# Optimization experiments

Measured on AMD Instinct MI355X. Metric: run time of the kernel, lower is better.

The kernel has to match this reference:

```python
import jax, jax.numpy as jnp
import numpy as np

NORMAL, INFLOW, OUTFLOW, WALL, PRESS_POINT = 0, 4, 5, 6, 7
NX = NY = 1024


def setup_inputs() -> dict:
    Ex, Ey = NX + 2, NY + 2
    n = NX * NY
    n_ext = Ex * Ey
    oidx = np.arange(n); io = oidx % NX; jo = oidx // NX
    nt = np.zeros(n, np.int32)
    nt[jo == 0] = WALL; nt[jo == NY - 1] = WALL
    nt[io == 0] = INFLOW; nt[io == NX - 1] = OUTFLOW
    e = np.arange(n_ext); ie = e % Ex; je = e // Ex
    extend_index = (np.clip(je - 1, 0, NY - 1) * NX + np.clip(ie - 1, 0, NX - 1)).astype(np.int32)
    ent = nt[extend_index].copy()
    ent[je == 0] = WALL; ent[je == Ey - 1] = WALL
    ent[ie == 0] = INFLOW; ent[ie == Ex - 1] = OUTFLOW
    ent[(Ey // 2) * Ex + Ex // 2] = PRESS_POINT
    jr = np.arange(1, Ey - 1); ir = np.arange(1, Ex - 1)
    ghost = np.concatenate([
        np.stack([jr * Ex, jr * Ex + 1, jr * Ex + 2], 1),
        np.stack([jr * Ex + Ex - 1, jr * Ex + Ex - 2, jr * Ex + Ex - 3], 1),
        np.stack([ir, Ex + ir, 2 * Ex + ir], 1),
        np.stack([(Ey - 1) * Ex + ir, (Ey - 2) * Ex + ir, (Ey - 3) * Ex + ir], 1)], 0).astype(np.int32)
    fx = np.arange((Ex - 1) * Ey); fxi = fx % (Ex - 1); fxj = fx // (Ex - 1)
    edge_node_xi = np.stack([fxj * Ex + fxi, fxj * Ex + fxi + 1], 0).astype(np.int32)
    fy = np.arange(Ex * (Ey - 1)); fyi = fy % Ex; fyj = fy // Ex
    edge_node_eta = np.stack([fyj * Ex + fyi, (fyj + 1) * Ex + fyi], 0).astype(np.int32)
    ie0 = io + 1; je0 = jo + 1
    xi_face = np.stack([je0 * (Ex - 1) + ie0 - 1, je0 * (Ex - 1) + ie0], 0).astype(np.int32)
    eta_face = np.stack([(je0 - 1) * Ex + ie0, je0 * Ex + ie0], 0).astype(np.int32)
    c = np.arange((Ex - 1) * (Ey - 1)); ci = c % (Ex - 1); cj = c // (Ex - 1)
    block_cells_node = np.stack([cj * Ex + ci, cj * Ex + ci + 1, (cj + 1) * Ex + ci, (cj + 1) * Ex + ci + 1], 0).astype(np.int32)
    xi_cell_index = np.stack([fyj * (Ex - 1) + np.clip(fyi - 1, 0, Ex - 2), fyj * (Ex - 1) + np.clip(fyi, 0, Ex - 2)], 0).astype(np.int32)
    key = jax.random.key(0)
    k = jax.random.split(key, 8)
    m0 = 1.0 + 0.05 * jax.random.normal(k[0], (n_ext,))
    m1 = 0.05 * jax.random.normal(k[1], (n_ext,))
    m2 = 0.05 * jax.random.normal(k[2], (n_ext,))
    m3 = 1.0 + 0.05 * jax.random.normal(k[3], (n_ext,))
    Jm = m0 * m3 - m1 * m2
    ebm = jnp.stack([m0, m1, m2, m3, Jm], 1)
    interior = (jo + 1) * Ex + (io + 1)
    obm = ebm[interior]
    return {
        "original_uv": 0.1 * jax.random.normal(k[4], (n, 3)),
        "uv_old": 0.1 * jax.random.normal(k[5], (n, 3)),
        "node_y": 0.1 * jax.random.normal(k[6], (n, 3)),
        "original_block_metrics": obm,
        "extended_block_metrics": ebm,
        "dt_graph": jnp.full((1, 1), 0.01, jnp.float32),
        "pde_theta": 0.5 + jax.random.uniform(k[7], (1, 5)),
        "relaxtion": jnp.full((1, 1), 0.5, jnp.float32),
        "node_type": jnp.asarray(nt),
        "ext_node_type": jnp.asarray(ent),
        "extend_index": jnp.asarray(extend_index),
        "ghost_stencil": jnp.asarray(ghost),
        "block_cells_node": jnp.asarray(block_cells_node),
        "edge_node_xi": jnp.asarray(edge_node_xi),
        "edge_node_eta": jnp.asarray(edge_node_eta),
        "xi_face": jnp.asarray(xi_face),
        "eta_face": jnp.asarray(eta_face),
        "xi_cell_index": jnp.asarray(xi_cell_index),
        "batch": jnp.zeros((n,), jnp.int32),
    }


def _hard_enforce_bc(uvp, node_type, node_y, extend_index, ext_node_type, ghost):
    mask_bc = (node_type == INFLOW) | (node_type == WALL)
    out_mask = node_type == OUTFLOW
    dummy_uv = jnp.where(mask_bc[:, None], node_y[:, :2], uvp[:, :2])
    dummy_p = jnp.where(out_mask, 0.0, uvp[:, 2])
    dummy = jnp.concatenate([dummy_uv, dummy_p[:, None]], 1)
    dummy_ext = dummy[extend_index]
    ext = uvp[extend_index]
    g0, g1, g2 = ghost[:, 0], ghost[:, 1], ghost[:, 2]
    gt = ext_node_type[g0]
    uvmask = gt == OUTFLOW
    pmask = (gt == WALL) | (gt == INFLOW)
    new_uv = jnp.where(pmask[:, None], 2.0 * dummy_ext[g1, :2] - ext[g2, :2],
                       jnp.where(uvmask[:, None], ext[g2, :2], ext[g0, :2]))
    new_p = jnp.where(uvmask, 2.0 * dummy_ext[g1, 2] - ext[g2, 2],
                      jnp.where(pmask, ext[g2, 2], ext[g0, 2]))
    return ext.at[g0, :2].set(new_uv).at[g0, 2].set(new_p)


def _convect_flux(uv, dxx, dxy, dex, dey, Jm, ln, rn, dn, un, le, re, de, ue):
    U = (uv[:, 0] * dxx + uv[:, 1] * dxy) / Jm
    V = (uv[:, 0] * dex + uv[:, 1] * dey) / Jm
    U_face = 0.5 * (U[ln] + U[rn]); V_face = 0.5 * (V[dn] + V[un])
    uv_xi = 0.5 * (uv[ln] + uv[rn]); uv_eta = 0.5 * (uv[dn] + uv[un])
    d1 = uv_xi[re] * U_face[re][:, None] - uv_xi[le] * U_face[le][:, None]
    d2 = uv_eta[ue] * V_face[ue][:, None] - uv_eta[de] * V_face[de][:, None]
    return jnp.concatenate([d1, d2], 1)  # [n,4]: dE1u,dE1v,dE2u,dE2v


def _diffuse_flux(uv, dxx, dxy, dex, dey, Jm, ln, rn, dn, un, le, re, de, ue):
    # central second-difference viscous flux in curvilinear coords (orthogonal terms)
    a11 = (dxx * dxx + dxy * dxy) / Jm
    a22 = (dex * dex + dey * dey) / Jm
    fx = (0.5 * (a11[ln] + a11[rn]))[:, None] * (uv[rn] - uv[ln])
    fy = (0.5 * (a22[dn] + a22[un]))[:, None] * (uv[un] - uv[dn])
    return jnp.concatenate([fx[re] - fx[le], fy[ue] - fy[de]], 1)


def _forward(original_uv, uv_old, node_y, obm, ebm, dt_graph, pde_theta, relaxtion,
             node_type, ext_node_type, extend_index, ghost_stencil, block_cells_node,
             edge_node_xi, edge_node_eta, xi_face, eta_face, xi_cell_index, batch):
    ext_old = _hard_enforce_bc(uv_old, node_type, node_y, extend_index, ext_node_type, ghost_stencil)
    ext = _hard_enforce_bc(original_uv, node_type, node_y, extend_index, ext_node_type, ghost_stencil)
    press = ext_node_type == PRESS_POINT
    ext = ext.at[:, 2].set(jnp.where(press, 0.0, ext[:, 2]))
    dxx, dxy, dex, dey, Jm = ebm[:, 0], ebm[:, 1], ebm[:, 2], ebm[:, 3], ebm[:, 4]
    J_o = obm[:, 4]
    ln, rn = edge_node_xi[0], edge_node_xi[1]
    dn, un = edge_node_eta[0], edge_node_eta[1]
    le, re = xi_face[0], xi_face[1]
    de, ue = eta_face[0], eta_face[1]
    lc, rc = xi_cell_index[0], xi_cell_index[1]
    dt_node = dt_graph[batch]            # [n,1]
    theta = pde_theta[batch]             # [n,5]
    uc, cc, convc, pc, dc = theta[:, 0:1], theta[:, 1:2], theta[:, 2:3], theta[:, 3:4], theta[:, 4:5]
    relax = relaxtion[batch]             # [n,1]
    uvc = ext[:, :2]; p = ext[:, 2]
    # continuity
    U = (uvc[:, 0] * dxx + uvc[:, 1] * dxy) / Jm
    V = (uvc[:, 0] * dex + uvc[:, 1] * dey) / Jm
    U_face = 0.5 * (U[ln] + U[rn]); V_face = 0.5 * (V[dn] + V[un])
    loss_cont = (U_face[re] - U_face[le] + V_face[ue] - V_face[de])[:, None] * cc
    conv_old = _convect_flux(ext_old[:, :2], dxx, dxy, dex, dey, Jm, ln, rn, dn, un, le, re, de, ue)
    conv_new = _convect_flux(uvc, dxx, dxy, dex, dey, Jm, ln, rn, dn, un, le, re, de, ue)
    diff_new = _diffuse_flux(uvc, dxx, dxy, dex, dey, Jm, ln, rn, dn, un, le, re, de, ue)
    conv = conv_old * relax + conv_new * (1.0 - relax)
    dE1u, dE1v, dE2u, dE2v = conv[:, 0], conv[:, 1], conv[:, 2], conv[:, 3]
    dv1u, dv1v, dv2u, dv2v = diff_new[:, 0], diff_new[:, 1], diff_new[:, 2], diff_new[:, 3]
    # pressure gradient
    pq = p / Jm
    pxx = pq * dxx; pxy = pq * dxy; pex = pq * dex; pey = pq * dey
    pxx_f = 0.5 * (pxx[ln] + pxx[rn]); pxy_f = 0.5 * (pxy[ln] + pxy[rn])
    pex_f = 0.5 * (pex[dn] + pex[un]); pey_f = 0.5 * (pey[dn] + pey[un])
    gPx = pxx_f[re] - pxx_f[le] + pex_f[ue] - pex_f[de]
    gPy = pey_f[ue] - pey_f[de] + pxy_f[re] - pxy_f[le]
    convect = jnp.stack([dE1u + dE2u, dE1v + dE2v], 1)
    diffusion = jnp.stack([dv1u + dv2u, dv1v + dv2v], 1)
    unsteady = (original_uv[:, :2] - uv_old[:, :2]) / dt_node / J_o[:, None]
    grad_P = jnp.stack([gPx, gPy], 1)
    momentum = uc * unsteady + convc * convect + pc * grad_P - dc * diffusion
    # smooth=True visualization field
    cell_uvp = 0.25 * (ext[block_cells_node[0]] + ext[block_cells_node[1]] + ext[block_cells_node[2]] + ext[block_cells_node[3]])
    face_eta = 0.5 * (cell_uvp[lc] + cell_uvp[rc])
    uvp_to_vis = jax.lax.stop_gradient(0.5 * (face_eta[ue] + face_eta[de]))
    return loss_cont, momentum[:, 0:1], momentum[:, 1:2], uvp_to_vis


def reference(original_uv, uv_old, node_y, original_block_metrics, extended_block_metrics,
              dt_graph, pde_theta, relaxtion, node_type, ext_node_type, extend_index,
              ghost_stencil, block_cells_node, edge_node_xi, edge_node_eta, xi_face,
              eta_face, xi_cell_index, batch):
    return _forward(original_uv, uv_old, node_y, original_block_metrics, extended_block_metrics,
                    dt_graph, pde_theta, relaxtion, node_type, ext_node_type, extend_index,
                    ghost_stencil, block_cells_node, edge_node_xi, edge_node_eta, xi_face,
                    eta_face, xi_cell_index, batch)
```

## Files before the change

kernel.cpp:

```cpp
#include <hip/hip_runtime.h>


#define NXC 1024
#define EXC 1026
#define NN  (NXC*NXC)

enum { T_NORMAL=0, T_INFLOW=4, T_OUTFLOW=5, T_WALL=6, T_PRESS=7 };

struct V3 { float u,v,p; };

__device__ __forceinline__ int ntype(int io,int jo){
  if (io==NXC-1) return T_OUTFLOW;
  if (io==0)     return T_INFLOW;
  if (jo==0 || jo==NXC-1) return T_WALL;
  return T_NORMAL;
}

template<bool NEWF>
__device__ __forceinline__ V3 ext_at(int je,int ie,
    const float* __restrict__ uvp,
    const float* __restrict__ node_y)
{
  V3 r;
  const bool bl=(ie==0), br=(ie==EXC-1), bb=(je==0), bt=(je==EXC-1);
  const bool onx = bl||br, ony = bb||bt;
  const bool ghost = (onx && !ony) || (ony && !onx);
  if (!ghost){
    int io = ie-1; io = io<0?0:(io>NXC-1?NXC-1:io);
    int jo = je-1; jo = jo<0?0:(jo>NXC-1?NXC-1:jo);
    int m3 = 3*(jo*NXC+io);
    r.u = uvp[m3]; r.v = uvp[m3+1]; r.p = uvp[m3+2];
    if (NEWF && je==EXC/2 && ie==EXC/2) r.p = 0.f;
    return r;
  }
  int dje=0, die=0, gt;
  if (bl)      { die= 1; gt=T_INFLOW;  }
  else if (br) { die=-1; gt=T_OUTFLOW; }
  else if (bb) { dje= 1; gt=T_WALL;    }
  else         { dje=-1; gt=T_WALL;    }
  int io1 = ie+die-1, jo1 = je+dje-1;
  int m1 = 3*(jo1*NXC+io1);
  int m2 = 3*((jo1+dje)*NXC + (io1+die));
  float u2=uvp[m2], v2=uvp[m2+1], p2=uvp[m2+2];
  int nt1 = ntype(io1,jo1);
  if (gt==T_OUTFLOW){
    float p1 = (nt1==T_OUTFLOW) ? 0.f : uvp[m1+2];
    r.u=u2; r.v=v2; r.p = 2.f*p1 - p2;
  } else {
    float du,dv;
    if (nt1==T_INFLOW || nt1==T_WALL){ du=node_y[m1]; dv=node_y[m1+1]; }
    else                             { du=uvp[m1];    dv=uvp[m1+1];    }
    r.u = 2.f*du - u2; r.v = 2.f*dv - v2; r.p = p2;
  }
  return r;
}

__device__ void process_slow(int io,int jo,
    const float* __restrict__ uvp, const float* __restrict__ uvo,
    const float* __restrict__ ndy, const float* __restrict__ ebm,
    float dt,float uc,float cc,float convc,float pc,float dc,float relax,
    float* __restrict__ out)
{
  const int o = jo*NXC + io;
  const int ie0 = io+1, je0 = jo+1;
  V3 C  = ext_at<true >(je0,  ie0,  uvp, ndy);
  V3 W  = ext_at<true >(je0,  ie0-1,uvp, ndy);
  V3 E  = ext_at<true >(je0,  ie0+1,uvp, ndy);
  V3 S  = ext_at<true >(je0-1,ie0,  uvp, ndy);
  V3 Nn = ext_at<true >(je0+1,ie0,  uvp, ndy);
  V3 SW = ext_at<true >(je0-1,ie0-1,uvp, ndy);
  V3 SE = ext_at<true >(je0-1,ie0+1,uvp, ndy);
  V3 NW = ext_at<true >(je0+1,ie0-1,uvp, ndy);
  V3 NE = ext_at<true >(je0+1,ie0+1,uvp, ndy);
  V3 Co = ext_at<false>(je0,  ie0,  uvo, ndy);
  V3 Wo = ext_at<false>(je0,  ie0-1,uvo, ndy);
  V3 Eo = ext_at<false>(je0,  ie0+1,uvo, ndy);
  V3 So = ext_at<false>(je0-1,ie0,  uvo, ndy);
  V3 No = ext_at<false>(je0+1,ie0,  uvo, ndy);

  const int eC = je0*EXC+ie0;
  const int eW = eC-1, eE = eC+1, eS = eC-EXC, eN = eC+EXC;
  float dxxC=ebm[5*eC+0], dxyC=ebm[5*eC+1], dexC=ebm[5*eC+2],
        deyC=ebm[5*eC+3], JmC=ebm[5*eC+4];
  float dxxW=ebm[5*eW+0], dxyW=ebm[5*eW+1], JmW=ebm[5*eW+4];
  float dxxE=ebm[5*eE+0], dxyE=ebm[5*eE+1], JmE=ebm[5*eE+4];
  float dexS=ebm[5*eS+2], deyS=ebm[5*eS+3], JmS=ebm[5*eS+4];
  float dexN=ebm[5*eN+2], deyN=ebm[5*eN+3], JmN=ebm[5*eN+4];
  const float rC=1.f/JmC, rW=1.f/JmW, rE=1.f/JmE, rS=1.f/JmS, rN=1.f/JmN;

  float UC=(C.u*dxxC + C.v*dxyC)*rC, UW=(W.u*dxxW + W.v*dxyW)*rW, UE=(E.u*dxxE + E.v*dxyE)*rE;
  float VC=(C.u*dexC + C.v*deyC)*rC, VS=(S.u*dexS + S.v*deyS)*rS, VN=(Nn.u*dexN + Nn.v*deyN)*rN;
  float UCo=(Co.u*dxxC + Co.v*dxyC)*rC, UWo=(Wo.u*dxxW + Wo.v*dxyW)*rW, UEo=(Eo.u*dxxE + Eo.v*dxyE)*rE;
  float VCo=(Co.u*dexC + Co.v*deyC)*rC, VSo=(So.u*dexS + So.v*deyS)*rS, VNo=(No.u*dexN + No.v*deyN)*rN;

  float Ufl =0.5f*(UW +UC ), Ufr =0.5f*(UC +UE );
  float Vfd =0.5f*(VS +VC ), Vfu =0.5f*(VC +VN );
  float Uflo=0.5f*(UWo+UCo), Ufro=0.5f*(UCo+UEo);
  float Vfdo=0.5f*(VSo+VCo), Vfuo=0.5f*(VCo+VNo);

  const float loss = (Ufr - Ufl + Vfu - Vfd) * cc;

  float cnu = 0.5f*(C.u+E.u)*Ufr - 0.5f*(W.u+C.u)*Ufl + 0.5f*(C.u+Nn.u)*Vfu - 0.5f*(S.u+C.u)*Vfd;
  float cnv = 0.5f*(C.v+E.v)*Ufr - 0.5f*(W.v+C.v)*Ufl + 0.5f*(C.v+Nn.v)*Vfu - 0.5f*(S.v+C.v)*Vfd;
  float cou = 0.5f*(Co.u+Eo.u)*Ufro - 0.5f*(Wo.u+Co.u)*Uflo + 0.5f*(Co.u+No.u)*Vfuo - 0.5f*(So.u+Co.u)*Vfdo;
  float cov = 0.5f*(Co.v+Eo.v)*Ufro - 0.5f*(Wo.v+Co.v)*Uflo + 0.5f*(Co.v+No.v)*Vfuo - 0.5f*(So.v+Co.v)*Vfdo;
  const float convu = relax*cou + (1.f-relax)*cnu;
  const float convv = relax*cov + (1.f-relax)*cnv;

  float a11C=(dxxC*dxxC+dxyC*dxyC)*rC, a11W=(dxxW*dxxW+dxyW*dxyW)*rW, a11E=(dxxE*dxxE+dxyE*dxyE)*rE;
  float a22C=(dexC*dexC+deyC*deyC)*rC, a22S=(dexS*dexS+deyS*deyS)*rS, a22N=(dexN*dexN+deyN*deyN)*rN;
  float du = 0.5f*(a11C+a11E)*(E.u -C.u) - 0.5f*(a11W+a11C)*(C.u-W.u)
           + 0.5f*(a22C+a22N)*(Nn.u-C.u) - 0.5f*(a22S+a22C)*(C.u-S.u);
  float dv = 0.5f*(a11C+a11E)*(E.v -C.v) - 0.5f*(a11W+a11C)*(C.v-W.v)
           + 0.5f*(a22C+a22N)*(Nn.v-C.v) - 0.5f*(a22S+a22C)*(C.v-S.v);

  float pqW=W.p*rW, pqE=E.p*rE, pqS=S.p*rS, pqN=Nn.p*rN;
  const float gPx = 0.5f*(pqE*dxxE - pqW*dxxW) + 0.5f*(pqN*dexN - pqS*dexS);
  const float gPy = 0.5f*(pqN*deyN - pqS*deyS) + 0.5f*(pqE*dxyE - pqW*dxyW);

  const float rdt = 1.f/dt;
  const float unst_u = (C.u - Co.u)*rdt*rC;
  const float unst_v = (C.v - Co.v)*rdt*rC;

  const float momu = uc*unst_u + convc*convu + pc*gPx - dc*du;
  const float momv = uc*unst_v + convc*convv + pc*gPy - dc*dv;

  const float visu = (SW.u+SE.u+NW.u+NE.u + 2.f*(S.u+W.u+E.u+Nn.u) + 4.f*C.u)*0.0625f;
  const float visv = (SW.v+SE.v+NW.v+NE.v + 2.f*(S.v+W.v+E.v+Nn.v) + 4.f*C.v)*0.0625f;
  const float visp = (SW.p+SE.p+NW.p+NE.p + 2.f*(S.p+W.p+E.p+Nn.p) + 4.f*C.p)*0.0625f;

  out[o]        = loss;
  out[NN + o]   = momu;
  out[2*NN + o] = momv;
  const int vb = 3*NN + 3*o;
  out[vb]   = visu;
  out[vb+1] = visv;
  out[vb+2] = visp;
}

extern "C" __global__ void __launch_bounds__(512)
fd_kernel(const float* __restrict__ uvp,
          const float* __restrict__ uvo,
          const float* __restrict__ ndy,
          const float* __restrict__ ebm,
          const float* __restrict__ dtg,
          const float* __restrict__ th,
          const float* __restrict__ rl,
          float* __restrict__ out)
{
  const int jo = blockIdx.x;
  int t = threadIdx.x;
  int s = (t==63) ? 511 : ((t==511) ? 63 : t);
  const int x0 = s*2;

  const float dt   = dtg[0];
  const float uc   = th[0], cc = th[1], convc = th[2], pc = th[3], dc = th[4];
  const float relax= rl[0];
  const float rdt  = 1.f/dt;

  const bool edge = (x0==0) | (x0==NXC-2) | (jo==0) | (jo==NXC-1);
  if (edge){
    process_slow(x0,  jo, uvp,uvo,ndy,ebm, dt,uc,cc,convc,pc,dc,relax, out);
    process_slow(x0+1,jo, uvp,uvo,ndy,ebm, dt,uc,cc,convc,pc,dc,relax, out);
    return;
  }

  const int rm=jo-1, rc=jo, rp=jo+1;

  float nS[12], nC[12], nN[12];
  {
    const float* a = uvp + 3*(rm*NXC + x0-1);
    const float* b = uvp + 3*(rc*NXC + x0-1);
    const float* c = uvp + 3*(rp*NXC + x0-1);
    #pragma unroll
    for (int k=0;k<12;k++){ nS[k]=a[k]; nC[k]=b[k]; nN[k]=c[k]; }
  }
  float qS[6], qC[12], qN[6];
  {
    const float* a = uvo + 3*(rm*NXC + x0);
    const float* b = uvo + 3*(rc*NXC + x0-1);
    const float* c = uvo + 3*(rp*NXC + x0);
    #pragma unroll
    for (int k=0;k<6;k++){ qS[k]=a[k]; qN[k]=c[k]; }
    #pragma unroll
    for (int k=0;k<12;k++){ qC[k]=b[k]; }
  }
  float mc[20], ms[10], mn[10];
  {
    const float* a = ebm + 5*((jo  )*EXC + x0+1);
    const float* b = ebm + 5*((jo+1)*EXC + x0);
    const float* c = ebm + 5*((jo+2)*EXC + x0+1);
    #pragma unroll
    for (int k=0;k<10;k++){ ms[k]=a[k]; mn[k]=c[k]; }
    #pragma unroll
    for (int k=0;k<20;k++){ mc[k]=b[k]; }
  }

  {
    const int c = 513 - x0;
    if ((unsigned)c < 4u){
      if (rm==512) nS[3*c+2]=0.f;
      if (rc==512) nC[3*c+2]=0.f;
      if (rp==512) nN[3*c+2]=0.f;
    }
  }

  float Un[4],Uo[4],a11[4],pqx[4],pqy[4],rJ[4],dex_[4],dey_[4];
  #pragma unroll
  for (int k=0;k<4;k++){
    const float dxx=mc[5*k], dxy=mc[5*k+1];
    dex_[k]=mc[5*k+2]; dey_[k]=mc[5*k+3];
    rJ[k]=1.f/mc[5*k+4];
    Un[k]=(nC[3*k]*dxx + nC[3*k+1]*dxy)*rJ[k];
    Uo[k]=(qC[3*k]*dxx + qC[3*k+1]*dxy)*rJ[k];
    a11[k]=(dxx*dxx+dxy*dxy)*rJ[k];
    const float pr = nC[3*k+2]*rJ[k];
    pqx[k]=pr*dxx; pqy[k]=pr*dxy;
  }
  float Vc[2],Voc[2],a22c[2];
  #pragma unroll
  for (int i=0;i<2;i++){
    const int m=1+i;
    Vc[i] =(nC[3*m]*dex_[m] + nC[3*m+1]*dey_[m])*rJ[m];
    Voc[i]=(qC[3*m]*dex_[m] + qC[3*m+1]*dey_[m])*rJ[m];
    a22c[i]=(dex_[m]*dex_[m]+dey_[m]*dey_[m])*rJ[m];
  }
  float VnS[2],VoS[2],a22S[2],pexS[2],peyS[2];
  float VnN[2],VoN[2],a22N[2],pexN[2],peyN[2];
  #pragma unroll
  for (int i=0;i<2;i++){
    const int m=1+i;
    {
      const float de=ms[5*i+2], dn=ms[5*i+3], r=1.f/ms[5*i+4];
      VnS[i]=(nS[3*m]*de + nS[3*m+1]*dn)*r;
      VoS[i]=(qS[3*i]*de + qS[3*i+1]*dn)*r;
      a22S[i]=(de*de+dn*dn)*r;
      const float pr=nS[3*m+2]*r;
      pexS[i]=pr*de; peyS[i]=pr*dn;
    }
    {
      const float de=mn[5*i+2], dn=mn[5*i+3], r=1.f/mn[5*i+4];
      VnN[i]=(nN[3*m]*de + nN[3*m+1]*dn)*r;
      VoN[i]=(qN[3*i]*de + qN[3*i+1]*dn)*r;
      a22N[i]=(de*de+dn*dn)*r;
      const float pr=nN[3*m+2]*r;
      pexN[i]=pr*de; peyN[i]=pr*dn;
    }
  }

  const int o0 = jo*NXC + x0;
  float Lo[2],Mu[2],Mv[2],Vu[2],Vv[2],Vp[2];
  #pragma unroll
  for (int i=0;i<2;i++){
    const int m=1+i;
    const float Ufl =0.5f*(Un[m-1]+Un[m]), Ufr =0.5f*(Un[m]+Un[m+1]);
    const float Uflo=0.5f*(Uo[m-1]+Uo[m]), Ufro=0.5f*(Uo[m]+Uo[m+1]);
    const float Vfd =0.5f*(VnS[i]+Vc[i]),  Vfu =0.5f*(Vc[i]+VnN[i]);
    const float Vfdo=0.5f*(VoS[i]+Voc[i]), Vfuo=0.5f*(Voc[i]+VoN[i]);

    Lo[i] = (Ufr - Ufl + Vfu - Vfd) * cc;

    const float u_c=nC[3*m],   v_c=nC[3*m+1];
    const float uW =nC[3*m-3], vW =nC[3*m-2];
    const float uE =nC[3*m+3], vE =nC[3*m+4];
    const float uS =nS[3*m],   vS =nS[3*m+1];
    const float uN =nN[3*m],   vN =nN[3*m+1];

    const float cnu = 0.5f*(u_c+uE)*Ufr - 0.5f*(uW+u_c)*Ufl
                    + 0.5f*(u_c+uN)*Vfu - 0.5f*(uS+u_c)*Vfd;
    const float cnv = 0.5f*(v_c+vE)*Ufr - 0.5f*(vW+v_c)*Ufl
                    + 0.5f*(v_c+vN)*Vfu - 0.5f*(vS+v_c)*Vfd;

    const float uoc=qC[3*m],   voc=qC[3*m+1];
    const float uoW=qC[3*m-3], voW=qC[3*m-2];
    const float uoE=qC[3*m+3], voE=qC[3*m+4];
    const float uoS=qS[3*i],   voS=qS[3*i+1];
    const float uoN=qN[3*i],   voN=qN[3*i+1];

    const float cou = 0.5f*(uoc+uoE)*Ufro - 0.5f*(uoW+uoc)*Uflo
                    + 0.5f*(uoc+uoN)*Vfuo - 0.5f*(uoS+uoc)*Vfdo;
    const float cov = 0.5f*(voc+voE)*Ufro - 0.5f*(voW+voc)*Uflo
                    + 0.5f*(voc+voN)*Vfuo - 0.5f*(voS+voc)*Vfdo;

    const float convu = relax*cou + (1.f-relax)*cnu;
    const float convv = relax*cov + (1.f-relax)*cnv;

    const float du = 0.5f*(a11[m]+a11[m+1])*(uE-u_c) - 0.5f*(a11[m-1]+a11[m])*(u_c-uW)
                   + 0.5f*(a22c[i]+a22N[i])*(uN-u_c) - 0.5f*(a22S[i]+a22c[i])*(u_c-uS);
    const float dv = 0.5f*(a11[m]+a11[m+1])*(vE-v_c) - 0.5f*(a11[m-1]+a11[m])*(v_c-vW)
                   + 0.5f*(a22c[i]+a22N[i])*(vN-v_c) - 0.5f*(a22S[i]+a22c[i])*(v_c-vS);

    const float gPx = 0.5f*(pqx[m+1]-pqx[m-1]) + 0.5f*(pexN[i]-pexS[i]);
    const float gPy = 0.5f*(peyN[i]-peyS[i]) + 0.5f*(pqy[m+1]-pqy[m-1]);

    const float unst_u = (u_c - uoc)*rdt*rJ[m];
    const float unst_v = (v_c - voc)*rdt*rJ[m];

    Mu[i] = uc*unst_u + convc*convu + pc*gPx - dc*du;
    Mv[i] = uc*unst_v + convc*convv + pc*gPy - dc*dv;

    Vu[i] = (nS[3*m-3]+2.f*nS[3*m]+nS[3*m+3]
       +2.f*(nC[3*m-3]+2.f*nC[3*m]+nC[3*m+3])
           + nN[3*m-3]+2.f*nN[3*m]+nN[3*m+3])*0.0625f;
    Vv[i] = (nS[3*m-2]+2.f*nS[3*m+1]+nS[3*m+4]
       +2.f*(nC[3*m-2]+2.f*nC[3*m+1]+nC[3*m+4])
           + nN[3*m-2]+2.f*nN[3*m+1]+nN[3*m+4])*0.0625f;
    Vp[i] = (nS[3*m-1]+2.f*nS[3*m+2]+nS[3*m+5]
       +2.f*(nC[3*m-1]+2.f*nC[3*m+2]+nC[3*m+5])
           + nN[3*m-1]+2.f*nN[3*m+2]+nN[3*m+5])*0.0625f;
  }

  out[o0]          = Lo[0]; out[o0+1]        = Lo[1];
  out[NN+o0]       = Mu[0]; out[NN+o0+1]     = Mu[1];
  out[2*NN+o0]     = Mv[0]; out[2*NN+o0+1]   = Mv[1];
  const int vb = 3*NN + 3*o0;
  out[vb]   = Vu[0]; out[vb+1] = Vv[0]; out[vb+2] = Vp[0];
  out[vb+3] = Vu[1]; out[vb+4] = Vv[1]; out[vb+5] = Vp[1];
}

extern "C" void kernel_launch(void* const* d_in, const int* in_sizes, int n_in,
                              void* d_out, int out_size, void* d_ws, size_t ws_size,
                              hipStream_t stream) {
  const float* uvp = (const float*)d_in[0];
  const float* uvo = (const float*)d_in[1];
  const float* ndy = (const float*)d_in[2];
  const float* ebm = (const float*)d_in[4];
  const float* dtg = (const float*)d_in[5];
  const float* th  = (const float*)d_in[6];
  const float* rl  = (const float*)d_in[7];
  float* out = (float*)d_out;

  fd_kernel<<<dim3(NXC), dim3(512), 0, stream>>>(uvp, uvo, ndy, ebm, dtg, th, rl, out);
}
```

Baseline: 197.3 us.

## Move boundary points to dedicated blocks and tile interior in 2D

Boundary nodes (top and bottom rows, plus the two outermost columns on each side) now go to a small set of dedicated blocks, one point per thread, using the slow path. Interior nodes use the fast path over 128x8 tiles instead of one block per row. This removes the divergent mixed edge/interior warps and the whole-row slow blocks, and gives neighbouring rows better cache locality. In exchange it adds index remapping and some idle threads in the last row tiles.

```diff
diff --git a/kernel.cpp b/kernel.cpp
--- a/kernel.cpp
+++ b/kernel.cpp
@@ -138,6 +138,8 @@
   out[vb+2] = visp;
 }
 
+#define NEDGE_BLK 12
+
 extern "C" __global__ void __launch_bounds__(512)
 fd_kernel(const float* __restrict__ uvp,
           const float* __restrict__ uvo,
@@ -148,52 +150,60 @@
           const float* __restrict__ rl,
           float* __restrict__ out)
 {
-  const int jo = blockIdx.x;
-  int t = threadIdx.x;
-  int s = (t==63) ? 511 : ((t==511) ? 63 : t);
-  const int x0 = s*2;
+  const int bid = blockIdx.x;
+  const int tid = threadIdx.x;
 
   const float dt   = dtg[0];
   const float uc   = th[0], cc = th[1], convc = th[2], pc = th[3], dc = th[4];
   const float relax= rl[0];
   const float rdt  = 1.f/dt;
 
-  const bool edge = (x0==0) | (x0==NXC-2) | (jo==0) | (jo==NXC-1);
-  if (edge){
-    process_slow(x0,  jo, uvp,uvo,ndy,ebm, dt,uc,cc,convc,pc,dc,relax, out);
-    process_slow(x0+1,jo, uvp,uvo,ndy,ebm, dt,uc,cc,convc,pc,dc,relax, out);
+  if (bid < NEDGE_BLK){
+    const int t = bid*512 + tid;
+    if (t >= 6136) return;
+    int io, jo;
+    if (t < 2048){ jo = (t < 1024) ? 0 : 1023; io = t & 1023; }
+    else { int u = t - 2048; jo = 1 + (u >> 2); int c = u & 3; io = (c < 2) ? c : 1020 + c; }
+    process_slow(io, jo, uvp,uvo,ndy,ebm, dt,uc,cc,convc,pc,dc,relax, out);
     return;
   }
+
+  const int b  = bid - NEDGE_BLK;
+  const int ct = b & 7, rt = b >> 3;
+  const int tx = tid & 63, ty = tid >> 6;
+  const int x0 = 2 + ct*128 + 2*tx;
+  const int jo = 1 + rt*8 + ty;
+  if (x0 > 1020 || jo > 1022) return;
 
   const int rm=jo-1, rc=jo, rp=jo+1;
 
   float nS[12], nC[12], nN[12];
   {
     const float* a = uvp + 3*(rm*NXC + x0-1);
-    const float* b = uvp + 3*(rc*NXC + x0-1);
+    const float* b2 = uvp + 3*(rc*NXC + x0-1);
     const float* c = uvp + 3*(rp*NXC + x0-1);
     #pragma unroll
-    for (int k=0;k<12;k++){ nS[k]=a[k]; nC[k]=b[k]; nN[k]=c[k]; }
+    for (int k=0;k<12;k++){ nS[k]=a[k]; nC[k]=b2[k]; nN[k]=c[k]; }
   }
   float qS[6], qC[12], qN[6];
   {
     const float* a = uvo + 3*(rm*NXC + x0);
-    const float* b = uvo + 3*(rc*NXC + x0-1);
+    const float* b2 = uvo + 3*(rc*NXC + x0-1);
     const float* c = uvo + 3*(rp*NXC + x0);
     #pragma unroll
     for (int k=0;k<6;k++){ qS[k]=a[k]; qN[k]=c[k]; }
     #pragma unroll
-    for (int k=0;k<12;k++){ qC[k]=b[k]; }
+    for (int k=0;k<12;k++){ qC[k]=b2[k]; }
   }
   float mc[20], ms[10], mn[10];
   {
     const float* a = ebm + 5*((jo  )*EXC + x0+1);
-    const float* b = ebm + 5*((jo+1)*EXC + x0);
+    const float* b2 = ebm + 5*((jo+1)*EXC + x0);
     const float* c = ebm + 5*((jo+2)*EXC + x0+1);
     #pragma unroll
     for (int k=0;k<10;k++){ ms[k]=a[k]; mn[k]=c[k]; }
     #pragma unroll
-    for (int k=0;k<20;k++){ mc[k]=b[k]; }
+    for (int k=0;k<20;k++){ mc[k]=b2[k]; }
   }
 
   {
@@ -330,5 +340,5 @@
   const float* rl  = (const float*)d_in[7];
   float* out = (float*)d_out;
 
-  fd_kernel<<<dim3(NXC), dim3(512), 0, stream>>>(uvp, uvo, ndy, ebm, dtg, th, rl, out);
-}
+  fd_kernel<<<dim3(NEDGE_BLK + 1024), dim3(512), 0, stream>>>(uvp, uvo, ndy, ebm, dtg, th, rl, out);
+}
```

Measured after the change: 182.0 us. -7.8%, faster.
